# Performance work log

Hardware: AMD Instinct MI355X
Metric: run time of the kernel (lower is better)

The kernel has to match this reference:

```python
import jax, jax.numpy as jnp
import numpy as np

SHIFT = 8  # shift_range init kwarg
EPS = 1e-12  # F.normalize default eps (x / max(||x||, eps))


def setup_inputs() -> dict:
    key = jax.random.key(0)
    k1, k2 = jax.random.split(key)
    grd_feature = jax.random.normal(k1, (64, 64, 24, 24), dtype=jnp.float32)
    sat_feature = jax.random.normal(k2, (64, 64, 64, 64), dtype=jnp.float32)
    return {"grd_feature": grd_feature, "sat_feature": sat_feature}


def reference(grd_feature, sat_feature):
    M, C, Hs, Ws = sat_feature.shape
    N, _, H, W = grd_feature.shape
    kH = min(H, Hs - 2 * SHIFT, 24)
    kW = min(W, Ws - 2 * SHIFT, 24)
    # center-crop ground features to kernel size
    grd = grd_feature[:, :, H // 2 - kH // 2: H // 2 + kH // 2,
                      W // 2 - kW // 2: W // 2 + kW // 2]  # [N,C,kH,kW]
    # crop sat features to search window (kernel + 2*shift)
    sat = sat_feature[:, :, Hs // 2 - SHIFT - kH // 2: Hs // 2 + SHIFT + kH // 2,
                      Ws // 2 - SHIFT - kW // 2: Ws // 2 + SHIFT + kW // 2]  # [M,C,Hi,Wi]
    # cross-correlation: repeat+grouped-conv in torch == plain conv2d here -> [M,N,Ho,Wo]
    corr = jax.lax.conv_general_dilated(
        sat, grd, window_strides=(1, 1), padding='VALID',
        dimension_numbers=('NCHW', 'OIHW', 'NCHW'))
    Ho, Wo = corr.shape[2], corr.shape[3]
    flat_idx = jnp.argmax(corr.reshape(M, N, Ho * Wo), axis=-1)  # [M,N]
    hy = flat_idx // Wo
    wx = flat_idx % Wo

    def gather_patch(sat_j, h, w):  # sat_j: [C,Hi,Wi]
        return jax.lax.dynamic_slice(sat_j, (0, h, w), (C, kH, kW))

    # vectorized patch gather over (M, N) -> [M,N,C,kH,kW]
    patches = jax.vmap(
        lambda sj, hs, ws: jax.vmap(lambda h, w: gather_patch(sj, h, w))(hs, ws)
    )(sat, hy, wx)

    pn = patches.reshape(M * N, -1)
    pn = pn / jnp.maximum(jnp.linalg.norm(pn, axis=-1, keepdims=True), EPS)
    pn = pn.reshape(M, N, C, kH, kW)
    gn = grd.reshape(N, -1)
    gn = gn / jnp.maximum(jnp.linalg.norm(gn, axis=-1, keepdims=True), EPS)
    gn = gn.reshape(N, C, kH, kW)
    similarity_matrix = jnp.einsum('mnchw,nchw->mn', pn, gn)
    sat_f = patches[M - 1, N - 1]  # last gathered (unnormalized) patch, as in torch
    return similarity_matrix, sat_f
```

## Files before the change

### kernel.cpp

```cpp
#include <hip/hip_runtime.h>
#include <hip/hip_bf16.h>
#include <math.h>


typedef float f32x16 __attribute__((ext_vector_type(16)));
typedef short short8 __attribute__((ext_vector_type(8)));

#define SATT_H 0u
#define GRDT_H 3276800u
#define CORR_O 4456448u
#define WIN2_O 5701632u
#define GN2_O  5720128u
#define IDX_O  5720192u
#define CEX_O  5721216u

__global__ __launch_bounds__(256) void make_satT(const float* __restrict__ sat,
                                                 __hip_bfloat16* __restrict__ sth) {
    __shared__ __hip_bfloat16 th[40 * 66];
    int m = blockIdx.x / 40, r = blockIdx.x % 40;
    int tid = threadIdx.x;
    const float* base = sat + (size_t)m * 262144 + (12 + r) * 64 + 12;
    for (int k = 0; k < 10; k++) {
        int idx = tid + 256 * k;
        int c = idx / 40, w2 = idx % 40;
        th[w2 * 66 + c] = __float2bfloat16(base[c * 4096 + w2]);
    }
    __syncthreads();
    __hip_bfloat16* dh = sth + (size_t)m * 102400;
    for (int k = 0; k < 10; k++) {
        int idx = tid + 256 * k;
        int w2 = idx >> 6, c = idx & 63;
        dh[(c >> 4) * 25600 + (r * 40 + w2) * 16 + (c & 15)] = th[w2 * 66 + c];
    }
}

__global__ __launch_bounds__(256) void make_grdT(const float* __restrict__ grd,
                                                 __hip_bfloat16* __restrict__ gth,
                                                 float* __restrict__ gn2) {
    __shared__ __hip_bfloat16 t[32 * 577];
    __shared__ float red[4];
    int bid = blockIdx.x;
    int n = bid >> 1, ch = bid & 1;
    int tid = threadIdx.x;
    const float* src = grd + (size_t)n * 36864 + ch * 32 * 576;
    float s = 0.0f;
    for (int k = 0; k < 72; k++) {
        int idx = tid + 256 * k;
        int cl = idx / 576, ij = idx % 576;
        float v = src[idx];
        s += v * v;
        t[cl * 577 + ij] = __float2bfloat16(v);
    }
    for (int off = 32; off; off >>= 1) s += __shfl_down(s, off);
    if ((tid & 63) == 0) red[tid >> 6] = s;
    __syncthreads();
    if (tid == 0) atomicAdd(&gn2[n], red[0] + red[1] + red[2] + red[3]);
    for (int k = 0; k < 72; k++) {
        int idx = tid + 256 * k;
        int ij = idx >> 5, cl = idx & 31;
        int c = ch * 32 + cl;
        gth[((size_t)((c >> 4) * 576 + ij)) * 1024 + n * 16 + (c & 15)] = t[cl * 577 + ij];
    }
}

__global__ __launch_bounds__(256) void make_win2(const __hip_bfloat16* __restrict__ sth,
                                                 float* __restrict__ win2) {
    __shared__ float S2[40][41];
    __shared__ float RS[40][18];
    int m = blockIdx.x, tid = threadIdx.x;
    const __hip_bfloat16* base = sth + (size_t)m * 102400;
    for (int k = 0; k < 7; k++) {
        int pix = tid + 256 * k;
        if (pix < 1600) {
            float s = 0.0f;
            for (int cc = 0; cc < 4; cc++) {
                const __hip_bfloat16* p = base + cc * 25600 + pix * 16;
                for (int cl = 0; cl < 16; cl++) {
                    float v = __bfloat162float(p[cl]);
                    s += v * v;
                }
            }
            S2[pix / 40][pix % 40] = s;
        }
    }
    __syncthreads();
    for (int k = 0; k < 3; k++) {
        int idx = tid + 256 * k;
        if (idx < 680) {
            int r = idx / 17, x = idx % 17;
            float s = 0.0f;
            for (int j = 0; j < 24; j++) s += S2[r][x + j];
            RS[r][x] = s;
        }
    }
    __syncthreads();
    for (int k = 0; k < 2; k++) {
        int idx = tid + 256 * k;
        if (idx < 289) {
            int y = idx / 17, x = idx % 17;
            float s = 0.0f;
            for (int i2 = 0; i2 < 24; i2++) s += RS[y + i2][x];
            win2[m * 289 + idx] = s;
        }
    }
}

__global__ __launch_bounds__(256, 2) void corr_mfma(const __hip_bfloat16* __restrict__ sth,
                                                    const __hip_bfloat16* __restrict__ gth,
                                                    float* __restrict__ corr) {
    __shared__ __align__(16) __hip_bfloat16 satW[760 * 16];
    __shared__ __align__(16) __hip_bfloat16 Bl[2][6][64 * 16];

    int bid = blockIdx.x;
    int xcd = bid & 7, slot = bid >> 3;
    int m = xcd * 8 + (slot >> 3), iq = slot & 7;
    int tid = threadIdx.x;
    int w = tid >> 6, l = tid & 63;
    int ln31 = l & 31, h = l >> 5;

    int rowbase[3];
#pragma unroll
    for (int t = 0; t < 3; t++) {
        int p = (w + 4 * t) * 32 + ln31;
        if (p > 288) p = 288;
        rowbase[t] = (p / 17) * 40 + (p % 17);
    }
    f32x16 acc[3][2];
#pragma unroll
    for (int t = 0; t < 3; t++) {
        acc[t][0] = (f32x16)0.0f;
        acc[t][1] = (f32x16)0.0f;
    }

    int glb = tid >> 7;
    int wi  = tid & 127;

#define BLOAD(d0, d1, d2, CC, G) {                                              \
        size_t pb = ((size_t)(CC) * 576 + iq * 72 + 6 * (G) + glb) * 1024 + wi * 8; \
        d0 = *(const float4*)(gth + pb);                                        \
        d1 = *(const float4*)(gth + pb + 2048);                                 \
        d2 = *(const float4*)(gth + pb + 4096);                                 \
    }
#define BWRITE(BUF, v0, v1, v2) {                                               \
        char* bb = (char*)&Bl[BUF][0][0] + glb * 2048 + wi * 16;                \
        *(float4*)bb = v0;                                                      \
        *(float4*)(bb + 4096) = v1;                                             \
        *(float4*)(bb + 8192) = v2;                                             \
    }

#pragma unroll
    for (int cc = 0; cc < 4; cc++) {
        __syncthreads();
        const __hip_bfloat16* satb = sth + (size_t)m * 102400 + cc * 25600 + iq * 1920;
#pragma unroll
        for (int k2 = 0; k2 < 6; k2++) {
            int s = tid + 256 * k2;
            if (s < 1520) {
                float4 v = *(const float4*)(satb + s * 8);
                *(float4*)((char*)satW + s * 16) = v;
            }
        }
        float4 b0, b1, b2;
        BLOAD(b0, b1, b2, cc, 0);
        BWRITE(0, b0, b1, b2);
        BLOAD(b0, b1, b2, cc, 1);
        __syncthreads();

        for (int g = 0; g < 12; g++) {
            int buf = g & 1;
            if (g + 1 < 12) {
                BWRITE(buf ^ 1, b0, b1, b2);
                if (g + 2 < 12) BLOAD(b0, b1, b2, cc, g + 2);
            }
#pragma unroll
            for (int ii = 0; ii < 6; ii++) {
                int ijl = 6 * g + ii;
                int il = ijl / 24;
                int pixoff = il * 40 + (ijl - il * 24);
                const char* blp = (const char*)&Bl[buf][ii][0];
                short8 bf0 = *(const short8*)(blp + ln31 * 32 + h * 16);
                short8 bf1 = *(const short8*)(blp + 1024 + ln31 * 32 + h * 16);
                if (w < 2) {
#pragma unroll
                    for (int t = 0; t < 3; t++) {
                        int ao = (rowbase[t] + pixoff) * 32 + h * 16;
                        short8 af = *(const short8*)((const char*)satW + ao);
                        acc[t][0] = __builtin_amdgcn_mfma_f32_32x32x16_bf16(af, bf0, acc[t][0], 0, 0, 0);
                        acc[t][1] = __builtin_amdgcn_mfma_f32_32x32x16_bf16(af, bf1, acc[t][1], 0, 0, 0);
                    }
                } else {
#pragma unroll
                    for (int t = 0; t < 2; t++) {
                        int ao = (rowbase[t] + pixoff) * 32 + h * 16;
                        short8 af = *(const short8*)((const char*)satW + ao);
                        acc[t][0] = __builtin_amdgcn_mfma_f32_32x32x16_bf16(af, bf0, acc[t][0], 0, 0, 0);
                        acc[t][1] = __builtin_amdgcn_mfma_f32_32x32x16_bf16(af, bf1, acc[t][1], 0, 0, 0);
                    }
                }
            }
            __syncthreads();
        }
    }

    int T = (w < 2) ? 3 : 2;
#pragma unroll
    for (int t = 0; t < 3; t++) {
        if (t >= T) break;
        int tile = w + 4 * t;
#pragma unroll
        for (int nt = 0; nt < 2; nt++)
#pragma unroll
            for (int q = 0; q < 16; q++) {
                int prow = tile * 32 + (q & 3) + 8 * (q >> 2) + 4 * h;
                if (prow < 289)
                    atomicAdd(&corr[((size_t)m * 304 + prow) * 64 + nt * 32 + ln31],
                              acc[t][nt][q]);
            }
    }
#undef BLOAD
#undef BWRITE
}

__global__ __launch_bounds__(64) void argsim(const float* __restrict__ corr,
                                             const float* __restrict__ win2,
                                             const float* __restrict__ gn2,
                                             float* __restrict__ out,
                                             int* __restrict__ idxb) {
    int b = blockIdx.x, m = b >> 6, n = b & 63, lane = threadIdx.x;
    float bv = -3.0e38f;
    int bi = 1 << 30;
    for (int k = 0; k < 5; k++) {
        int p = lane + 64 * k;
        if (p < 289) {
            float v = corr[((size_t)m * 304 + p) * 64 + n];
            if (v > bv) { bv = v; bi = p; }
        }
    }
    for (int off = 32; off; off >>= 1) {
        float ov = __shfl_down(bv, off);
        int oi = __shfl_down(bi, off);
        if (ov > bv || (ov == bv && oi < bi)) { bv = ov; bi = oi; }
    }
    if (lane == 0) {
        float np = sqrtf(win2[m * 289 + bi]);
        float ng = sqrtf(gn2[n]);
        out[b] = bv / (fmaxf(np, 1e-12f) * fmaxf(ng, 1e-12f));
        idxb[b] = bi;
    }
}

__global__ __launch_bounds__(256) void exact63(const float* __restrict__ sat,
                                               const float* __restrict__ grd,
                                               float* __restrict__ correx) {
    int p = blockIdx.x;
    int hy = p / 17, wx = p % 17;
    int tid = threadIdx.x;
    const float* satm = sat + (size_t)63 * 262144;
    const float* grdn = grd + (size_t)63 * 36864;
    float dot = 0.0f;
    for (int e = tid; e < 36864; e += 256) {
        int c = e / 576, rem = e - c * 576;
        int i = rem / 24, j = rem - i * 24;
        dot += satm[c * 4096 + (12 + hy + i) * 64 + 12 + wx + j] * grdn[e];
    }
    for (int off = 32; off; off >>= 1) dot += __shfl_down(dot, off);
    __shared__ float red[4];
    if ((tid & 63) == 0) red[tid >> 6] = dot;
    __syncthreads();
    if (tid == 0) correx[p] = red[0] + red[1] + red[2] + red[3];
}

__global__ __launch_bounds__(64) void fix63(const float* __restrict__ correx,
                                            const float* __restrict__ win2,
                                            const float* __restrict__ gn2,
                                            float* __restrict__ out,
                                            int* __restrict__ idxb) {
    int lane = threadIdx.x;
    float bv = -3.0e38f;
    int bi = 1 << 30;
    for (int k = 0; k < 5; k++) {
        int p = lane + 64 * k;
        if (p < 289) {
            float v = correx[p];
            if (v > bv) { bv = v; bi = p; }
        }
    }
    for (int off = 32; off; off >>= 1) {
        float ov = __shfl_down(bv, off);
        int oi = __shfl_down(bi, off);
        if (ov > bv || (ov == bv && oi < bi)) { bv = ov; bi = oi; }
    }
    if (lane == 0) {
        out[4095] = bv / (fmaxf(sqrtf(win2[63 * 289 + bi]), 1e-12f) *
                          fmaxf(sqrtf(gn2[63]), 1e-12f));
        idxb[4095] = bi;
    }
}

__global__ __launch_bounds__(256) void copy_patch(const float* __restrict__ sat,
                                                  const int* __restrict__ idxb,
                                                  float* __restrict__ out) {
    int fidx = idxb[4095];
    int hy = fidx / 17, wx = fidx % 17;
    int e = blockIdx.x * 256 + threadIdx.x;
    int c = e / 576;
    int rem = e - c * 576;
    int rr = rem / 24, col = rem - rr * 24;
    out[4096 + e] = sat[(size_t)(63 * 64 + c) * 4096 + (12 + hy + rr) * 64 + 12 + wx + col];
}

extern "C" void kernel_launch(void* const* d_in, const int* in_sizes, int n_in,
                              void* d_out, int out_size, void* d_ws, size_t ws_size,
                              hipStream_t stream) {
    const float* grd = (const float*)d_in[0];
    const float* sat = (const float*)d_in[1];
    float* out = (float*)d_out;

    float* wsf = (float*)d_ws;
    __hip_bfloat16* sth = (__hip_bfloat16*)(wsf + SATT_H);
    __hip_bfloat16* gth = (__hip_bfloat16*)(wsf + GRDT_H);
    float* corr = wsf + CORR_O;
    float* win2 = wsf + WIN2_O;
    float* gn2  = wsf + GN2_O;
    int*   idxb = (int*)(wsf + IDX_O);
    float* cex  = wsf + CEX_O;

    hipMemsetAsync(corr, 0, (size_t)1263744 * sizeof(float), stream);
    make_satT<<<2560, 256, 0, stream>>>(sat, sth);
    make_grdT<<<128, 256, 0, stream>>>(grd, gth, gn2);
    make_win2<<<64, 256, 0, stream>>>(sth, win2);
    corr_mfma<<<512, 256, 0, stream>>>(sth, gth, corr);
    argsim<<<4096, 64, 0, stream>>>(corr, win2, gn2, out, idxb);
    exact63<<<289, 256, 0, stream>>>(sat, grd, cex);
    fix63<<<1, 64, 0, stream>>>(cex, win2, gn2, out, idxb);
    copy_patch<<<144, 256, 0, stream>>>(sat, idxb, out);
}
```

Measured before the change: 192.8 us.

## Load ground B fragments directly from global into registers, drop LDS double buffer

The correlation MFMA kernel no longer stages ground-feature B tiles through a double-buffered LDS array with per-group barriers. Each lane now loads its B fragments straight from global memory into registers, with a three-deep register rotation to prefetch ahead. This removes the LDS writes and reads and the 12 barriers per channel chunk. In exchange every wave fetches the same B data separately (more L2/global traffic), and load latency now has to be covered by the register prefetch alone. The make_satT store loop is also reordered so consecutive threads write contiguous 16-element runs.

```diff
diff --git a/kernel.cpp b/kernel.cpp
--- a/kernel.cpp
+++ b/kernel.cpp
@@ -26,11 +26,12 @@
         th[w2 * 66 + c] = __float2bfloat16(base[c * 4096 + w2]);
     }
     __syncthreads();
-    __hip_bfloat16* dh = sth + (size_t)m * 102400;
+    __hip_bfloat16* dh = sth + (size_t)m * 102400 + r * 640;
     for (int k = 0; k < 10; k++) {
         int idx = tid + 256 * k;
-        int w2 = idx >> 6, c = idx & 63;
-        dh[(c >> 4) * 25600 + (r * 40 + w2) * 16 + (c & 15)] = th[w2 * 66 + c];
+        int cc = idx / 640, rem = idx - cc * 640;
+        int w2 = rem >> 4, cl = rem & 15;
+        dh[cc * 25600 + w2 * 16 + cl] = th[w2 * 66 + cc * 16 + cl];
     }
 }
 
@@ -109,7 +110,6 @@
                                                     const __hip_bfloat16* __restrict__ gth,
                                                     float* __restrict__ corr) {
     __shared__ __align__(16) __hip_bfloat16 satW[760 * 16];
-    __shared__ __align__(16) __hip_bfloat16 Bl[2][6][64 * 16];
 
     int bid = blockIdx.x;
     int xcd = bid & 7, slot = bid >> 3;
@@ -132,20 +132,33 @@
         acc[t][1] = (f32x16)0.0f;
     }
 
-    int glb = tid >> 7;
-    int wi  = tid & 127;
-
-#define BLOAD(d0, d1, d2, CC, G) {                                              \
-        size_t pb = ((size_t)(CC) * 576 + iq * 72 + 6 * (G) + glb) * 1024 + wi * 8; \
-        d0 = *(const float4*)(gth + pb);                                        \
-        d1 = *(const float4*)(gth + pb + 2048);                                 \
-        d2 = *(const float4*)(gth + pb + 4096);                                 \
-    }
-#define BWRITE(BUF, v0, v1, v2) {                                               \
-        char* bb = (char*)&Bl[BUF][0][0] + glb * 2048 + wi * 16;                \
-        *(float4*)bb = v0;                                                      \
-        *(float4*)(bb + 4096) = v1;                                             \
-        *(float4*)(bb + 8192) = v2;                                             \
+    const __hip_bfloat16* gbase = gth + (size_t)(iq * 72) * 1024 + ln31 * 16 + h * 8;
+
+#define BLOADR(B0, B1, CC, IJL) {                                               \
+        const __hip_bfloat16* p_ = gbase + ((size_t)(CC) * 576 + (IJL)) * 1024; \
+        B0 = *(const short8*)p_;                                                \
+        B1 = *(const short8*)(p_ + 512);                                        \
+    }
+#define COMPUTE(IJL, B0, B1) {                                                  \
+        int il_ = (IJL) / 24;                                                   \
+        int pixoff_ = il_ * 40 + ((IJL) - il_ * 24);                            \
+        if (w < 2) {                                                            \
+            _Pragma("unroll")                                                   \
+            for (int t = 0; t < 3; t++) {                                       \
+                int ao = (rowbase[t] + pixoff_) * 32 + h * 16;                  \
+                short8 af = *(const short8*)((const char*)satW + ao);           \
+                acc[t][0] = __builtin_amdgcn_mfma_f32_32x32x16_bf16(af, B0, acc[t][0], 0, 0, 0); \
+                acc[t][1] = __builtin_amdgcn_mfma_f32_32x32x16_bf16(af, B1, acc[t][1], 0, 0, 0); \
+            }                                                                   \
+        } else {                                                                \
+            _Pragma("unroll")                                                   \
+            for (int t = 0; t < 2; t++) {                                       \
+                int ao = (rowbase[t] + pixoff_) * 32 + h * 16;                  \
+                short8 af = *(const short8*)((const char*)satW + ao);           \
+                acc[t][0] = __builtin_amdgcn_mfma_f32_32x32x16_bf16(af, B0, acc[t][0], 0, 0, 0); \
+                acc[t][1] = __builtin_amdgcn_mfma_f32_32x32x16_bf16(af, B1, acc[t][1], 0, 0, 0); \
+            }                                                                   \
+        }                                                                       \
     }
 
 #pragma unroll
@@ -160,45 +173,20 @@
                 *(float4*)((char*)satW + s * 16) = v;
             }
         }
-        float4 b0, b1, b2;
-        BLOAD(b0, b1, b2, cc, 0);
-        BWRITE(0, b0, b1, b2);
-        BLOAD(b0, b1, b2, cc, 1);
+        short8 x0, x1, y0, y1, z0, z1;
+        BLOADR(x0, x1, cc, 0);
+        BLOADR(y0, y1, cc, 1);
+        BLOADR(z0, z1, cc, 2);
         __syncthreads();
 
-        for (int g = 0; g < 12; g++) {
-            int buf = g & 1;
-            if (g + 1 < 12) {
-                BWRITE(buf ^ 1, b0, b1, b2);
-                if (g + 2 < 12) BLOAD(b0, b1, b2, cc, g + 2);
-            }
-#pragma unroll
-            for (int ii = 0; ii < 6; ii++) {
-                int ijl = 6 * g + ii;
-                int il = ijl / 24;
-                int pixoff = il * 40 + (ijl - il * 24);
-                const char* blp = (const char*)&Bl[buf][ii][0];
-                short8 bf0 = *(const short8*)(blp + ln31 * 32 + h * 16);
-                short8 bf1 = *(const short8*)(blp + 1024 + ln31 * 32 + h * 16);
-                if (w < 2) {
-#pragma unroll
-                    for (int t = 0; t < 3; t++) {
-                        int ao = (rowbase[t] + pixoff) * 32 + h * 16;
-                        short8 af = *(const short8*)((const char*)satW + ao);
-                        acc[t][0] = __builtin_amdgcn_mfma_f32_32x32x16_bf16(af, bf0, acc[t][0], 0, 0, 0);
-                        acc[t][1] = __builtin_amdgcn_mfma_f32_32x32x16_bf16(af, bf1, acc[t][1], 0, 0, 0);
-                    }
-                } else {
-#pragma unroll
-                    for (int t = 0; t < 2; t++) {
-                        int ao = (rowbase[t] + pixoff) * 32 + h * 16;
-                        short8 af = *(const short8*)((const char*)satW + ao);
-                        acc[t][0] = __builtin_amdgcn_mfma_f32_32x32x16_bf16(af, bf0, acc[t][0], 0, 0, 0);
-                        acc[t][1] = __builtin_amdgcn_mfma_f32_32x32x16_bf16(af, bf1, acc[t][1], 0, 0, 0);
-                    }
-                }
-            }
-            __syncthreads();
+        for (int ijg = 0; ijg < 24; ijg++) {
+            int base = ijg * 3;
+            COMPUTE(base + 0, x0, x1);
+            if (base + 3 < 72) BLOADR(x0, x1, cc, base + 3);
+            COMPUTE(base + 1, y0, y1);
+            if (base + 4 < 72) BLOADR(y0, y1, cc, base + 4);
+            COMPUTE(base + 2, z0, z1);
+            if (base + 5 < 72) BLOADR(z0, z1, cc, base + 5);
         }
     }
 
@@ -217,8 +205,8 @@
                               acc[t][nt][q]);
             }
     }
-#undef BLOAD
-#undef BWRITE
+#undef BLOADR
+#undef COMPUTE
 }
 
 __global__ __launch_bounds__(64) void argsim(const float* __restrict__ corr,
```

New measurement: 192.2 us. No clear change (-0.3%).
